# Optimization experiments

Measured on AMD Instinct MI355X. Metric: run time of the kernel, lower is better.

## Reference

```python
import jax, jax.numpy as jnp
import numpy as np

DIM = 768
HEADS = 8
HEAD_DIM = DIM // HEADS  # 96, divisible by 6 for 3-axis RoPE
ROPE_BASE = 10000.0


def rotary_pe_3d(x, coords):
    """Apply 3D-coordinate rotary embedding.
    x: [B, h, L, d] with d % 6 == 0; coords: [B, L, 3].
    Head dim is split into 3 equal blocks, one per spatial axis; each block
    gets rotate-half RoPE with angle = coord_axis * inv_freq.
    """
    B, h, L, d = x.shape
    d3 = d // 3
    half = d3 // 2
    inv_freq = 1.0 / (ROPE_BASE ** (jnp.arange(half, dtype=x.dtype) / half))  # [half]
    ang = coords[..., None] * inv_freq  # [B, L, 3, half]
    cos = jnp.cos(ang)[:, None]  # [B, 1, L, 3, half]
    sin = jnp.sin(ang)[:, None]
    xr = x.reshape(B, h, L, 3, d3)
    x1, x2 = xr[..., :half], xr[..., half:]
    out = jnp.concatenate([x1 * cos - x2 * sin, x1 * sin + x2 * cos], axis=-1)
    return out.reshape(B, h, L, d)


def setup_inputs() -> dict:
    key = jax.random.key(0)
    ks = jax.random.split(key, 9)
    B, Lq, Lk = 2, 2048, 2048
    s = DIM ** -0.5
    return {
        "Q_in": jax.random.normal(ks[0], (B, Lq, DIM), jnp.float32),
        "K_in": jax.random.normal(ks[1], (B, Lk, DIM), jnp.float32),
        "V_in": jax.random.normal(ks[2], (B, Lk, DIM), jnp.float32),
        "coords_q": jax.random.uniform(ks[3], (B, Lq, 3), jnp.float32) * 10.0,
        "coords_k": jax.random.uniform(ks[4], (B, Lk, 3), jnp.float32) * 10.0,
        "Wq": jax.random.normal(ks[5], (DIM, DIM), jnp.float32) * s,
        "Wk": jax.random.normal(ks[6], (DIM, DIM), jnp.float32) * s,
        "Wv": jax.random.normal(ks[7], (DIM, DIM), jnp.float32) * s,
        "Wo": jax.random.normal(ks[8], (DIM, DIM), jnp.float32) * s,
    }


def _split_heads(x, h):
    B, L, C = x.shape
    return x.reshape(B, L, h, C // h).transpose(0, 2, 1, 3)  # [B,h,L,d]


def reference(Q_in, K_in, V_in, coords_q, coords_k, Wq, Wk, Wv, Wo):
    scale = HEAD_DIM ** -0.5
    q = _split_heads(Q_in @ Wq.T, HEADS)
    k = _split_heads(K_in @ Wk.T, HEADS)
    v = _split_heads(V_in @ Wv.T, HEADS)
    q = rotary_pe_3d(q, coords_q)
    k = rotary_pe_3d(k, coords_k)
    attn = jnp.einsum('bhqd,bhkd->bhqk', q, k) * scale
    attn = jax.nn.softmax(attn, axis=-1)
    out = jnp.einsum('bhqk,bhkd->bhqd', attn, v)
    B, h, L, d = out.shape
    out = out.transpose(0, 2, 1, 3).reshape(B, L, h * d)
    return out @ Wo.T
```

## Files before the change

kernel.cpp:

```cpp
#include <hip/hip_runtime.h>
#include <stdint.h>

#define H 8
#define DH 96
#define L 2048
#define NB 2
#define D 768

typedef unsigned short u16;
typedef unsigned int u32;
typedef __attribute__((ext_vector_type(4))) __bf16 bf16x4;
typedef __attribute__((ext_vector_type(8))) __bf16 bf16x8;
typedef __attribute__((ext_vector_type(4))) float f32x4;
typedef __attribute__((ext_vector_type(16))) float f32x16;
typedef __attribute__((ext_vector_type(4))) u32 u32x4;
typedef __attribute__((ext_vector_type(2))) u32 u32x2;
typedef __attribute__((ext_vector_type(4))) u16 u16x4;

#define QSCALE 0.14724444f

static __device__ __forceinline__ u16 f2bf(float f) {
  union { __bf16 h; u16 u; } v;
  v.h = (__bf16)f;
  return v.u;
}

static __device__ __forceinline__ bf16x8 cvt8r(f32x4 a, f32x4 b) {
  bf16x8 r;
  r[0] = (__bf16)a[0]; r[1] = (__bf16)a[1]; r[2] = (__bf16)a[2]; r[3] = (__bf16)a[3];
  r[4] = (__bf16)b[0]; r[5] = (__bf16)b[1]; r[6] = (__bf16)b[2]; r[7] = (__bf16)b[3];
  return r;
}

static __device__ __forceinline__ void bar_lds() {
  asm volatile("s_waitcnt lgkmcnt(0)" ::: "memory");
  __builtin_amdgcn_s_barrier();
}

__global__ __launch_bounds__(256, 3)
void proj_qkv(const float* __restrict__ Qin, const float* __restrict__ Kin,
              const float* __restrict__ Vin,
              const float* __restrict__ Wq, const float* __restrict__ Wk,
              const float* __restrict__ Wv,
              const float* __restrict__ cq, const float* __restrict__ ck,
              u16* __restrict__ qo, u16* __restrict__ ko, u16* __restrict__ vo)
{
  __shared__ u16 a_lds[2][64 * 40];
  __shared__ u16 b_lds[2][192 * 40];
  const int tid = threadIdx.x;
  const int lane = tid & 63;
  const int w = tid >> 6;
  const int wr = w >> 1, wc = w & 1;
  const int fr = lane & 15;
  const int hi = lane >> 4;

  const int f = blockIdx.x;
  const int xcd = f & 7;
  const int g = f >> 3;
  const int bx = g & 3;
  const int h2 = g >> 2;
  const int byp = h2 & 7;
  const int z = h2 >> 3;
  const int by = xcd + 8 * byp;
  const int row0 = by * 64;
  const int col0 = bx * 192;

  const float* A = (z == 0) ? Qin : ((z == 1) ? Kin : Vin);
  const float* W = (z == 0) ? Wq : ((z == 1) ? Wk : Wv);

  const int arow = tid >> 2;
  const int acol = (tid & 3) * 8;
  const float* pA = A + (size_t)(row0 + arow) * D + acol;
  const float* pB0 = W + (size_t)(col0 + arow) * D + acol;
  const float* pB1 = pB0 + (size_t)64 * D;
  const float* pB2 = pB0 + (size_t)128 * D;

  f32x4 acc[2][6] = {};
  f32x4 Sa[2], Sb[6], Ta[2], Tb[6];

  auto issueP = [&](int k, f32x4* ra, f32x4* rb) {
    ra[0] = *(const f32x4*)(pA + k);
    ra[1] = *(const f32x4*)(pA + k + 4);
    rb[0] = *(const f32x4*)(pB0 + k);
    rb[1] = *(const f32x4*)(pB0 + k + 4);
    rb[2] = *(const f32x4*)(pB1 + k);
    rb[3] = *(const f32x4*)(pB1 + k + 4);
    rb[4] = *(const f32x4*)(pB2 + k);
    rb[5] = *(const f32x4*)(pB2 + k + 4);
  };
  auto stageP = [&](int bi, const f32x4* ra, const f32x4* rb) {
    *(bf16x8*)(&a_lds[bi][arow * 40 + acol]) = cvt8r(ra[0], ra[1]);
    *(bf16x8*)(&b_lds[bi][arow * 40 + acol]) = cvt8r(rb[0], rb[1]);
    *(bf16x8*)(&b_lds[bi][(arow + 64) * 40 + acol]) = cvt8r(rb[2], rb[3]);
    *(bf16x8*)(&b_lds[bi][(arow + 128) * 40 + acol]) = cvt8r(rb[4], rb[5]);
  };
  auto compute = [&](int bi) {
    bf16x8 af[2], bf[6];
#pragma unroll
    for (int m = 0; m < 2; m++)
      af[m] = *(const bf16x8*)(&a_lds[bi][(wr * 32 + m * 16 + fr) * 40 + hi * 8]);
#pragma unroll
    for (int n = 0; n < 6; n++)
      bf[n] = *(const bf16x8*)(&b_lds[bi][(wc * 96 + n * 16 + fr) * 40 + hi * 8]);
#pragma unroll
    for (int m = 0; m < 2; m++)
#pragma unroll
      for (int n = 0; n < 6; n++)
        acc[m][n] = __builtin_amdgcn_mfma_f32_16x16x32_bf16(af[m], bf[n], acc[m][n], 0, 0, 0);
  };

  issueP(0, Sa, Sb);
  stageP(0, Sa, Sb);
  issueP(32, Ta, Tb);
  bar_lds();

#pragma unroll 1
  for (int tt = 0; tt < 12; tt++) {
    const int k2 = tt * 64;
    if (k2 + 64 < D) issueP(k2 + 64, Sa, Sb);
    compute(0);
    stageP(1, Ta, Tb);
    bar_lds();
    if (k2 + 96 < D) issueP(k2 + 96, Ta, Tb);
    compute(1);
    if (k2 + 64 < D) stageP(0, Sa, Sb);
    bar_lds();
  }

  const int hh = (col0 + wc * 96) / DH;
  if (z == 2) {
#pragma unroll
    for (int m = 0; m < 2; m++) {
      int rbase = row0 + wr * 32 + m * 16 + hi * 4;
#pragma unroll
      for (int n = 0; n < 6; n++) {
        int dd = n * 16 + fr;
#pragma unroll
        for (int r = 0; r < 4; r++) {
          int row = rbase + r;
          int b = row >> 11, l = row & (L - 1);
          vo[((size_t)((b * H + hh) * DH + dd)) * L + l] = f2bf(acc[m][n][r]);
        }
      }
    }
  } else {
    const float* coords = (z == 0) ? cq : ck;
    u16* outp = (z == 0) ? qo : ko;
    const float postscale = (z == 0) ? QSCALE : 1.0f;
    const float invf = exp2f(-(float)fr * 0.83048202372184058f);
#pragma unroll
    for (int m = 0; m < 2; m++) {
      int rbase = row0 + wr * 32 + m * 16 + hi * 4;
#pragma unroll
      for (int np = 0; np < 3; np++) {
        int n1 = np * 2;
        int dd1 = n1 * 16 + fr;
#pragma unroll
        for (int r = 0; r < 4; r++) {
          int row = rbase + r;
          int b = row >> 11, l = row & (L - 1);
          float coord = coords[((size_t)(b * L + l)) * 3 + np];
          float ang = coord * invf;
          float sn = __sinf(ang), cs = __cosf(ang);
          float x1 = acc[m][n1][r], x2 = acc[m][n1 + 1][r];
          size_t base = ((size_t)((b * H + hh) * L + l)) * DH;
          outp[base + dd1] = f2bf((x1 * cs - x2 * sn) * postscale);
          outp[base + dd1 + 16] = f2bf((x1 * sn + x2 * cs) * postscale);
        }
      }
    }
  }
}

#define KSTR 104
#define VSTR 76
#define NT   (L / 64)
__global__ __launch_bounds__(256, 2)
void attn_fwd(const u16* __restrict__ q_ws, const u16* __restrict__ k_ws,
              const u16* __restrict__ vt_ws, u16* __restrict__ ao)
{
  __shared__ __attribute__((aligned(16))) u16 k_lds[2][64 * KSTR];
  __shared__ __attribute__((aligned(16))) u16 vt_lds[2][96 * VSTR];
  const int tid = threadIdx.x;
  const int lane = tid & 63;
  const int w = tid >> 6;

  const int f = blockIdx.x;
  const int xr = f & 7;
  const int g = f >> 3;
  const int qx = g & 31;
  const int bh = xr + 8 * (g >> 5);
  const int q0 = qx * 64;

  const int qlo = lane & 31;
  const int hi32 = lane >> 5;
  const int wq = w >> 1;
  const int kk0 = (w & 1) * 32;

  const u16* kbase = k_ws + (size_t)bh * L * DH;
  const u16* vtbase = vt_ws + (size_t)bh * DH * L;

  const int perm[4] = {0, 2, 1, 3};

  int kg_off[3], kl0[3], kl1[3];
  int vg_off[3], vl0[3], vl1[3];
#pragma unroll
  for (int it = 0; it < 3; it++) {
    int ch = tid + it * 256;
    int krow = ch / 12, dc = ch % 12;
    kg_off[it] = krow * DH + dc * 8;
    int c0 = dc * 2;
    kl0[it] = krow * KSTR + (c0 >> 2) * 16 + perm[c0 & 3] * 4;
    kl1[it] = krow * KSTR + (c0 >> 2) * 16 + perm[(c0 + 1) & 3] * 4;
    int vrow = ch >> 3, vq = (ch & 7) * 2;
    vg_off[it] = vrow * L + vq * 4;
    vl0[it] = vrow * VSTR + (vq >> 2) * 16 + perm[vq & 3] * 4;
    vl1[it] = vrow * VSTR + (vq >> 2) * 16 + perm[(vq + 1) & 3] * 4;
  }

  bf16x8 qf[6];
  {
    const u16* qb = q_ws + ((size_t)bh * L + q0 + wq * 32 + qlo) * DH;
#pragma unroll
    for (int s = 0; s < 6; s++) {
      bf16x4 a = *(const bf16x4*)(qb + s * 16 + hi32 * 4);
      bf16x4 b = *(const bf16x4*)(qb + s * 16 + hi32 * 4 + 8);
      bf16x8 q;
      q[0] = a[0]; q[1] = a[1]; q[2] = a[2]; q[3] = a[3];
      q[4] = b[0]; q[5] = b[1]; q[6] = b[2]; q[7] = b[3];
      qf[s] = q;
    }
  }

  f32x16 o[3] = {};
  float m_r = -1e30f, l_r = 0.f;

  u32x4 kreg[3], vreg[3];
  auto kissue = [&](int t) {
    const u16* kb = kbase + (size_t)t * 64 * DH;
    const u16* vb = vtbase + t * 64;
#pragma unroll
    for (int it = 0; it < 3; it++) {
      kreg[it] = *(const u32x4*)(kb + kg_off[it]);
      vreg[it] = *(const u32x4*)(vb + vg_off[it]);
    }
  };
  auto kwrite = [&](int bi) {
#pragma unroll
    for (int it = 0; it < 3; it++) {
      u32x2 klo = { kreg[it][0], kreg[it][1] };
      u32x2 khi = { kreg[it][2], kreg[it][3] };
      *(u32x2*)(&k_lds[bi][kl0[it]]) = klo;
      *(u32x2*)(&k_lds[bi][kl1[it]]) = khi;
      u32x2 vlo = { vreg[it][0], vreg[it][1] };
      u32x2 vhi = { vreg[it][2], vreg[it][3] };
      *(u32x2*)(&vt_lds[bi][vl0[it]]) = vlo;
      *(u32x2*)(&vt_lds[bi][vl1[it]]) = vhi;
    }
  };

  kissue(0);
  kwrite(0);
  __syncthreads();

  int cur = 0;
  for (int t = 0; t < NT; t++) {
    if (t + 1 < NT) kissue(t + 1);

    f32x16 s2 = {};
#pragma unroll
    for (int s = 0; s < 6; s++) {
      bf16x8 kfrag = *(const bf16x8*)(
          &k_lds[cur][(kk0 + qlo) * KSTR + s * 16 + hi32 * 8]);
      s2 = __builtin_amdgcn_mfma_f32_32x32x16_bf16(kfrag, qf[s], s2, 0, 0, 0);
    }

    float a0 = fmaxf(fmaxf(s2[0], s2[1]), s2[2]);
    float a1 = fmaxf(fmaxf(s2[3], s2[4]), s2[5]);
    float a2 = fmaxf(fmaxf(s2[6], s2[7]), s2[8]);
    float a3 = fmaxf(fmaxf(s2[9], s2[10]), s2[11]);
    float a4 = fmaxf(fmaxf(s2[12], s2[13]), s2[14]);
    float pmax = fmaxf(fmaxf(fmaxf(a0, a1), a2), fmaxf(fmaxf(a3, a4), s2[15]));
    if (!__all(pmax - m_r <= 8.0f)) {
      float mx = fmaxf(pmax, __shfl_xor(pmax, 32));
      float mn = fmaxf(m_r, mx);
      float alpha = exp2f(m_r - mn);
      m_r = mn;
      l_r *= alpha;
#pragma unroll
      for (int db = 0; db < 3; db++)
#pragma unroll
        for (int r = 0; r < 16; r++)
          o[db][r] *= alpha;
    }

    float p[16];
    float rs = 0.f;
#pragma unroll
    for (int r = 0; r < 16; r++) {
      p[r] = exp2f(s2[r] - m_r);
      rs += p[r];
    }
    l_r += rs;

    bf16x8 pt[2];
#pragma unroll
    for (int s = 0; s < 2; s++)
#pragma unroll
      for (int j = 0; j < 8; j++)
        pt[s][j] = (__bf16)p[s * 8 + j];

#pragma unroll
    for (int s = 0; s < 2; s++)
#pragma unroll
      for (int db = 0; db < 3; db++) {
        bf16x8 vfrag = *(const bf16x8*)(
            &vt_lds[cur][(db * 32 + qlo) * VSTR + kk0 + s * 16 + hi32 * 8]);
        o[db] = __builtin_amdgcn_mfma_f32_32x32x16_bf16(vfrag, pt[s], o[db], 0, 0, 0);
      }

    if (t + 1 < NT) {
      kwrite(cur ^ 1);
      __syncthreads();
      cur ^= 1;
    }
  }

  float l_w = l_r + __shfl_xor(l_r, 32);

  {
    float* xb = (float*)&k_lds[wq][0];
    const int base = lane * 52;
    if (w & 1) {
#pragma unroll
      for (int db = 0; db < 3; db++)
#pragma unroll
        for (int rg = 0; rg < 4; rg++) {
          f32x4 v = { o[db][rg * 4], o[db][rg * 4 + 1],
                      o[db][rg * 4 + 2], o[db][rg * 4 + 3] };
          *(f32x4*)&xb[base + db * 16 + rg * 4] = v;
        }
      xb[base + 48] = m_r;
      xb[base + 49] = l_w;
    }
    __syncthreads();
    if (!(w & 1)) {
      float m1 = xb[base + 48], l1 = xb[base + 49];
      float ms = fmaxf(m_r, m1);
      float c0 = exp2f(m_r - ms), c1 = exp2f(m1 - ms);
      float inv = 1.f / (l_w * c0 + l1 * c1);
      const int b = bh >> 3, hh = bh & 7;
      const int lrow = q0 + wq * 32 + qlo;
      u16* aop = ao + ((size_t)(b * L + lrow)) * D + hh * DH;
#pragma unroll
      for (int db = 0; db < 3; db++)
#pragma unroll
        for (int rg = 0; rg < 4; rg++) {
          f32x4 op = *(const f32x4*)&xb[base + db * 16 + rg * 4];
          u16x4 pk;
#pragma unroll
          for (int r4 = 0; r4 < 4; r4++)
            pk[r4] = f2bf((o[db][rg * 4 + r4] * c0 + op[r4] * c1) * inv);
          *(u16x4*)(aop + db * 32 + rg * 8 + hi32 * 4) = pk;
        }
    }
  }
}

__global__ __launch_bounds__(256, 3)
void gemm_out(const u16* __restrict__ A, const float* __restrict__ W,
              float* __restrict__ out)
{
  __shared__ u16 a_lds[2][64 * 40];
  __shared__ u16 b_lds[2][64 * 40];
  const int tid = threadIdx.x;
  const int lane = tid & 63;
  const int w = tid >> 6;
  const int wr = w >> 1, wc = w & 1;

  const int f = blockIdx.x;
  const int xr = f & 7;
  const int g = f >> 3;
  const int bx = g % 12;
  const int wq = g / 12;
  const int by = xr + 8 * wq;
  const int row0 = by * 64;
  const int col0 = bx * 64;

  f32x4 acc[2][2] = {};
  const int srow = tid >> 2;
  const int scol = (tid & 3) * 8;
  const u16* pA = A + (size_t)(row0 + srow) * D + scol;
  const float* pW = W + (size_t)(col0 + srow) * D + scol;
  const int fr = lane & 15;
  const int fk = (lane >> 4) * 8;

  auto issueG = [&](int k, u32x4* ra, f32x4* rb) {
    ra[0] = *(const u32x4*)(pA + k);
    rb[0] = *(const f32x4*)(pW + k);
    rb[1] = *(const f32x4*)(pW + k + 4);
  };
  auto writeG = [&](int bi, const u32x4* ra, const f32x4* rb) {
    *(u32x4*)(&a_lds[bi][srow * 40 + scol]) = ra[0];
    *(bf16x8*)(&b_lds[bi][srow * 40 + scol]) = cvt8r(rb[0], rb[1]);
  };
  auto computeG = [&](int bi) {
    bf16x8 af[2], bfr[2];
#pragma unroll
    for (int m = 0; m < 2; m++)
      af[m] = *(const bf16x8*)(&a_lds[bi][(wr * 32 + m * 16 + fr) * 40 + fk]);
#pragma unroll
    for (int n = 0; n < 2; n++)
      bfr[n] = *(const bf16x8*)(&b_lds[bi][(wc * 32 + n * 16 + fr) * 40 + fk]);
#pragma unroll
    for (int m = 0; m < 2; m++)
#pragma unroll
      for (int n = 0; n < 2; n++)
        acc[m][n] = __builtin_amdgcn_mfma_f32_16x16x32_bf16(af[m], bfr[n], acc[m][n], 0, 0, 0);
  };

  u32x4 raA[1], raB[1];
  f32x4 rbA[2], rbB[2];
  issueG(0, raB, rbB);
  writeG(0, raB, rbB);
  issueG(32, raA, rbA);
  __syncthreads();

  for (int k0 = 0; k0 < D; k0 += 64) {
    if (k0 + 64 < D) issueG(k0 + 64, raB, rbB);
    computeG(0);
    writeG(1, raA, rbA);
    __syncthreads();
    if (k0 + 96 < D) issueG(k0 + 96, raA, rbA);
    computeG(1);
    if (k0 + 64 < D) writeG(0, raB, rbB);
    __syncthreads();
  }

#pragma unroll
  for (int m = 0; m < 2; m++) {
    int rbase = row0 + wr * 32 + m * 16 + (lane >> 4) * 4;
#pragma unroll
    for (int n = 0; n < 2; n++) {
      int c = col0 + wc * 32 + n * 16 + fr;
#pragma unroll
      for (int r = 0; r < 4; r++)
        out[(size_t)(rbase + r) * D + c] = acc[m][n][r];
    }
  }
}

extern "C" void kernel_launch(void* const* d_in, const int* in_sizes, int n_in,
                              void* d_out, int out_size, void* d_ws, size_t ws_size,
                              hipStream_t stream) {
  (void)in_sizes; (void)n_in; (void)out_size;
  const float* Qin = (const float*)d_in[0];
  const float* Kin = (const float*)d_in[1];
  const float* Vin = (const float*)d_in[2];
  const float* cq  = (const float*)d_in[3];
  const float* ck  = (const float*)d_in[4];
  const float* Wq  = (const float*)d_in[5];
  const float* Wk  = (const float*)d_in[6];
  const float* Wv  = (const float*)d_in[7];
  const float* Wo  = (const float*)d_in[8];
  float* out = (float*)d_out;

  const size_t per = (size_t)NB * H * L * DH;
  if (ws_size < 4 * per * sizeof(u16)) return;

  u16* q_ws  = (u16*)d_ws;
  u16* k_ws  = q_ws + per;
  u16* vt_ws = k_ws + per;
  u16* ao_ws = vt_ws + per;

  proj_qkv<<<dim3(768), dim3(256), 0, stream>>>(
      Qin, Kin, Vin, Wq, Wk, Wv, cq, ck, q_ws, k_ws, vt_ws);
  attn_fwd<<<dim3(32 * NB * H), dim3(256), 0, stream>>>(q_ws, k_ws, vt_ws, ao_ws);
  gemm_out<<<dim3(12 * 64), dim3(256), 0, stream>>>(ao_ws, Wo, out);
}
```

Before: 98.16 us.

## Pre-convert QKV inputs and weights to bf16, then run DMA-fed projection GEMM

Adds a separate kernel that converts the three activation inputs and three weight matrices to bf16 in workspace scratch. A new projection kernel then streams the bf16 tiles straight into LDS with global_load_lds, using 128x128 tiles, and fuses RoPE, the Q scale and the V transpose into its epilogue. The old fp32-reading projection stays as a fallback when the workspace is too small. This adds an extra kernel launch and a full read/write pass over the inputs, and the main loop is single-buffered with two barriers per k step.

```diff
diff --git a/kernel.cpp b/kernel.cpp
--- a/kernel.cpp
+++ b/kernel.cpp
@@ -6,6 +6,8 @@
 #define L 2048
 #define NB 2
 #define D 768
+#define ACTE 3145728
+#define WELE 589824
 
 typedef unsigned short u16;
 typedef unsigned int u32;
@@ -35,6 +37,145 @@
 static __device__ __forceinline__ void bar_lds() {
   asm volatile("s_waitcnt lgkmcnt(0)" ::: "memory");
   __builtin_amdgcn_s_barrier();
+}
+
+__global__ __launch_bounds__(256)
+void cvt_bf16(const float* __restrict__ q, const float* __restrict__ k,
+              const float* __restrict__ v, const float* __restrict__ wq,
+              const float* __restrict__ wk, const float* __restrict__ wv,
+              u16* __restrict__ dst)
+{
+  const long NCH = (3L * ACTE + 3L * WELE) / 8;
+  for (long c = (long)blockIdx.x * 256 + threadIdx.x; c < NCH;
+       c += (long)gridDim.x * 256) {
+    long e = c * 8;
+    const float* s;
+    if (e < 3L * ACTE) {
+      int t = (int)(e / ACTE);
+      s = (t == 0 ? q : (t == 1 ? k : v)) + (e - (long)t * ACTE);
+    } else {
+      long e2 = e - 3L * ACTE;
+      int t = (int)(e2 / WELE);
+      s = (t == 0 ? wq : (t == 1 ? wk : wv)) + (e2 - (long)t * WELE);
+    }
+    f32x4 a = *(const f32x4*)s;
+    f32x4 b = *(const f32x4*)(s + 4);
+    *(bf16x8*)(dst + e) = cvt8r(a, b);
+  }
+}
+
+__global__ __launch_bounds__(256, 3)
+void proj_qkv_b(const u16* __restrict__ bfb,
+                const float* __restrict__ cq, const float* __restrict__ ck,
+                u16* __restrict__ qo, u16* __restrict__ ko, u16* __restrict__ vo)
+{
+  __shared__ __attribute__((aligned(16))) u16 a_lds[128 * 32];
+  __shared__ __attribute__((aligned(16))) u16 b_lds[128 * 32];
+  const int tid = threadIdx.x;
+  const int lane = tid & 63;
+  const int w = tid >> 6;
+  const int wr = w >> 1, wc = w & 1;
+  const int fr = lane & 15;
+  const int hi = lane >> 4;
+
+  const int f = blockIdx.x;
+  const int xr = f & 7;
+  const int g = f >> 3;
+  const int z = g / 24;
+  const int gg = g % 24;
+  const int by = xr + 8 * (gg & 3);
+  const int bx = gg >> 2;
+  const int row0 = by * 128;
+  const int col0 = bx * 128;
+
+  const u16* A = bfb + (size_t)z * ACTE;
+  const u16* W = bfb + 3L * ACTE + (size_t)z * WELE;
+
+  f32x4 acc[4][4] = {};
+
+  const int lrow = lane >> 2;
+  const int lcol = (lane & 3) * 8;
+  auto dma = [&](int k0) {
+#pragma unroll
+    for (int j = 0; j < 2; j++) {
+      const int r0 = w * 32 + j * 16;
+      const u16* gpa = A + (size_t)(row0 + r0 + lrow) * D + k0 + lcol;
+      const u16* gpb = W + (size_t)(col0 + r0 + lrow) * D + k0 + lcol;
+      __builtin_amdgcn_global_load_lds(
+          (const __attribute__((address_space(1))) u32*)gpa,
+          (__attribute__((address_space(3))) u32*)&a_lds[r0 * 32], 16, 0, 0);
+      __builtin_amdgcn_global_load_lds(
+          (const __attribute__((address_space(1))) u32*)gpb,
+          (__attribute__((address_space(3))) u32*)&b_lds[r0 * 32], 16, 0, 0);
+    }
+  };
+
+#pragma unroll 1
+  for (int k0 = 0; k0 < D; k0 += 32) {
+    dma(k0);
+    __syncthreads();
+    bf16x8 af[4], bf[4];
+#pragma unroll
+    for (int m = 0; m < 4; m++)
+      af[m] = *(const bf16x8*)(&a_lds[(wr * 64 + m * 16 + fr) * 32 + hi * 8]);
+#pragma unroll
+    for (int n = 0; n < 4; n++)
+      bf[n] = *(const bf16x8*)(&b_lds[(wc * 64 + n * 16 + fr) * 32 + hi * 8]);
+#pragma unroll
+    for (int m = 0; m < 4; m++)
+#pragma unroll
+      for (int n = 0; n < 4; n++)
+        acc[m][n] = __builtin_amdgcn_mfma_f32_16x16x32_bf16(af[m], bf[n], acc[m][n], 0, 0, 0);
+    __syncthreads();
+  }
+
+  if (z == 2) {
+#pragma unroll
+    for (int m = 0; m < 4; m++) {
+      int rbase = row0 + wr * 64 + m * 16 + hi * 4;
+#pragma unroll
+      for (int n = 0; n < 4; n++) {
+        int c = col0 + wc * 64 + n * 16 + fr;
+        int hh = c / DH, dd = c % DH;
+#pragma unroll
+        for (int r = 0; r < 4; r++) {
+          int row = rbase + r;
+          int b = row >> 11, l = row & (L - 1);
+          vo[((size_t)((b * H + hh) * DH + dd)) * L + l] = f2bf(acc[m][n][r]);
+        }
+      }
+    }
+  } else {
+    const float* coords = (z == 0) ? cq : ck;
+    u16* outp = (z == 0) ? qo : ko;
+    const float postscale = (z == 0) ? QSCALE : 1.0f;
+#pragma unroll
+    for (int m = 0; m < 4; m++) {
+      int rbase = row0 + wr * 64 + m * 16 + hi * 4;
+#pragma unroll
+      for (int np = 0; np < 2; np++) {
+        int n1 = np * 2;
+        int c1 = col0 + wc * 64 + n1 * 16 + fr;
+        int hh = c1 / DH;
+        int dd1 = c1 % DH;
+        int axis = dd1 / 32;
+        int j = dd1 & 15;
+        float invf = exp2f(-(float)j * 0.83048202372184058f);
+#pragma unroll
+        for (int r = 0; r < 4; r++) {
+          int row = rbase + r;
+          int b = row >> 11, l = row & (L - 1);
+          float coord = coords[((size_t)(b * L + l)) * 3 + axis];
+          float ang = coord * invf;
+          float sn = __sinf(ang), cs = __cosf(ang);
+          float x1 = acc[m][n1][r], x2 = acc[m][n1 + 1][r];
+          size_t base = ((size_t)((b * H + hh) * L + l)) * DH;
+          outp[base + dd1] = f2bf((x1 * cs - x2 * sn) * postscale);
+          outp[base + dd1 + 16] = f2bf((x1 * sn + x2 * cs) * postscale);
+        }
+      }
+    }
+  }
 }
 
 __global__ __launch_bounds__(256, 3)
@@ -466,15 +607,24 @@
   float* out = (float*)d_out;
 
   const size_t per = (size_t)NB * H * L * DH;
-  if (ws_size < 4 * per * sizeof(u16)) return;
+  const size_t base_need = 4 * per * sizeof(u16);
+  const size_t scr_elems = 3L * ACTE + 3L * WELE;
+  const size_t full_need = base_need + scr_elems * sizeof(u16);
+  if (ws_size < base_need) return;
 
   u16* q_ws  = (u16*)d_ws;
   u16* k_ws  = q_ws + per;
   u16* vt_ws = k_ws + per;
   u16* ao_ws = vt_ws + per;
 
-  proj_qkv<<<dim3(768), dim3(256), 0, stream>>>(
-      Qin, Kin, Vin, Wq, Wk, Wv, cq, ck, q_ws, k_ws, vt_ws);
+  if (ws_size >= full_need) {
+    u16* bfb = ao_ws + per;
+    cvt_bf16<<<dim3(2048), dim3(256), 0, stream>>>(Qin, Kin, Vin, Wq, Wk, Wv, bfb);
+    proj_qkv_b<<<dim3(576), dim3(256), 0, stream>>>(bfb, cq, ck, q_ws, k_ws, vt_ws);
+  } else {
+    proj_qkv<<<dim3(768), dim3(256), 0, stream>>>(
+        Qin, Kin, Vin, Wq, Wk, Wv, cq, ck, q_ws, k_ws, vt_ws);
+  }
   attn_fwd<<<dim3(32 * NB * H), dim3(256), 0, stream>>>(q_ws, k_ws, vt_ws, ao_ws);
   gemm_out<<<dim3(12 * 64), dim3(256), 0, stream>>>(ao_ws, Wo, out);
 }
```

Result: slower. 100.2 us (+2.1%).
